# Performance work log

Hardware: AMD Instinct MI355X
Metric: run time of the kernel (lower is better)

Reference implementation:

```python
import jax, jax.numpy as jnp
import numpy as np

N = 50000
E = 800000
IN_C, HID, HEADS, CLS = 128, 64, 5, 40
NEG_SLOPE = 0.2


def gat_conv(h, src, dst, W, a_src, a_dst, bias, heads, out_c, concat):
    n = h.shape[0]
    hp = (h @ W).reshape(n, heads, out_c)            # [N,H,C]
    a_s = jnp.sum(hp * a_src, axis=-1)               # [N,H]
    a_d = jnp.sum(hp * a_dst, axis=-1)               # [N,H]
    e = jax.nn.leaky_relu(a_s[src] + a_d[dst], NEG_SLOPE)  # [Etot,H]
    m = jax.ops.segment_max(e, dst, num_segments=n)  # segment softmax over dst
    e = jnp.exp(e - m[dst])
    s = jax.ops.segment_sum(e, dst, num_segments=n)
    alpha = e / (s[dst] + 1e-16)                     # [Etot,H]
    msg = hp[src] * alpha[:, :, None]                # [Etot,H,C]
    out = jax.ops.segment_sum(msg, dst, num_segments=n)
    if concat:
        out = out.reshape(n, heads * out_c)
    else:
        out = out.mean(axis=1)
    return out + bias


def setup_inputs() -> dict:
    key = jax.random.key(0)
    ks = jax.random.split(key, 12)
    x = jax.random.normal(ks[0], (N, IN_C), dtype=jnp.float32)
    edge_index = jax.random.randint(ks[1], (2, E), 0, N, dtype=jnp.int64)
    g = 0.1
    return {
        "x": x,
        "edge_index": edge_index,
        "emb_W": jax.random.normal(ks[2], (IN_C, HID), jnp.float32) * g,
        "emb_b": jnp.zeros((HID,), jnp.float32),
        "W1": jax.random.normal(ks[3], (HID, HEADS * HID), jnp.float32) * g,
        "att_src1": jax.random.normal(ks[4], (HEADS, HID), jnp.float32) * g,
        "att_dst1": jax.random.normal(ks[5], (HEADS, HID), jnp.float32) * g,
        "b1": jnp.zeros((HEADS * HID,), jnp.float32),
        "W2": jax.random.normal(ks[6], (HEADS * HID, HEADS * CLS), jnp.float32) * g,
        "att_src2": jax.random.normal(ks[7], (HEADS, CLS), jnp.float32) * g,
        "att_dst2": jax.random.normal(ks[8], (HEADS, CLS), jnp.float32) * g,
        "b2": jnp.zeros((CLS,), jnp.float32),
    }


def reference(x, edge_index, emb_W, emb_b, W1, att_src1, att_dst1, b1,
              W2, att_src2, att_dst2, b2):
    n = x.shape[0]
    loops = jnp.arange(n, dtype=edge_index.dtype)
    src = jnp.concatenate([edge_index[0], loops])  # PyG adds self-loops
    dst = jnp.concatenate([edge_index[1], loops])
    h = x @ emb_W + emb_b
    emb = h
    # dropout skipped (eval mode)
    h = jax.nn.elu(gat_conv(h, src, dst, W1, att_src1, att_dst1, b1, HEADS, HID, True))
    h = gat_conv(h, src, dst, W2, att_src2, att_dst2, b2, HEADS, CLS, False)
    return emb, jax.nn.log_softmax(h, axis=1)
```

## Files before the change

### kernel.cpp

```cpp
#include <hip/hip_runtime.h>
#include <math.h>

constexpr int N_NODES = 50000;
constexpr int E_EDGES = 800000;
constexpr int ETOT    = E_EDGES + N_NODES;
constexpr int IN_C    = 128;
constexpr int HID     = 64;
constexpr int HEADS   = 5;
constexpr int CLS     = 40;
constexpr int SLOTW   = 96;
constexpr int CSTR    = 16;
constexpr float NEG_SLOPE = 0.2f;

typedef __attribute__((ext_vector_type(8))) short short8;
typedef __attribute__((ext_vector_type(4))) float float4v;
typedef __attribute__((ext_vector_type(2))) float f32x2;

__device__ __forceinline__ float lrelu(float v) {
    return v > 0.f ? v : NEG_SLOPE * v;
}
__device__ __forceinline__ float bf2f(unsigned short u) {
    return __uint_as_float(((unsigned)u) << 16);
}
__device__ __forceinline__ f32x2 bfp2f(unsigned u) {
    f32x2 r;
    r.x = __uint_as_float(u << 16);
    r.y = __uint_as_float(u & 0xFFFF0000u);
    return r;
}
__device__ __forceinline__ unsigned short f2bf(float f) {
    unsigned u = __float_as_uint(f);
    return (unsigned short)((u + 0x7fffu + ((u >> 16) & 1u)) >> 16);
}

__device__ __forceinline__ void pack_one(const float* __restrict__ B,
                                         unsigned short* __restrict__ Bp,
                                         int N, int KS, int t)
{
    int lane = t & 63;
    int f = (t >> 6) & 3;
    int rest = t >> 8;
    int ks = rest % KS;
    int nt = rest / KS;
    int n = nt * 64 + f * 16 + (lane & 15);
    int kbase = ks * 32 + (lane >> 4) * 8;
    unsigned short vals[8];
    #pragma unroll
    for (int j = 0; j < 8; j++) {
        float v = (n < N) ? B[(long)(kbase + j) * N + n] : 0.f;
        vals[j] = f2bf(v);
    }
    *(ushort4*)(Bp + (long)t * 8)     = make_ushort4(vals[0], vals[1], vals[2], vals[3]);
    *(ushort4*)(Bp + (long)t * 8 + 4) = make_ushort4(vals[4], vals[5], vals[6], vals[7]);
}

__global__ void pack_weights(const float* __restrict__ W0, const float* __restrict__ W1,
                             const float* __restrict__ W2,
                             const float* __restrict__ att1s, const float* __restrict__ att1d,
                             const float* __restrict__ att2s, const float* __restrict__ att2d,
                             unsigned short* __restrict__ Bp0,
                             unsigned short* __restrict__ Bp1,
                             unsigned short* __restrict__ Bp2,
                             float* __restrict__ u1s, float* __restrict__ u1d,
                             unsigned short* __restrict__ Bs,
                             int* __restrict__ cnt, unsigned short* __restrict__ slots)
{
    int t = blockIdx.x * blockDim.x + threadIdx.x;
    if (t < 13824) {
        if (t < 1024)      pack_one(W0, Bp0, 64,  4,  t);
        else if (t < 3584) pack_one(W1, Bp1, 320, 2,  t - 1024);
        else               pack_one(W2, Bp2, 200, 10, t - 3584);
    } else if (t < 14464) {
        int i = t - 13824;
        bool isd = i >= 320;
        int j = isd ? i - 320 : i;
        int h = j >> 6, k = j & 63;
        const float* att = isd ? att1d : att1s;
        float sum = 0.f;
        for (int c = 0; c < 64; c++)
            sum += W1[k * 320 + h * 64 + c] * att[h * 64 + c];
        (isd ? u1d : u1s)[j] = sum;
    } else if (t < 15104) {
        int i = t - 14464;
        int lane = i & 63, ks = i >> 6;
        int n = lane & 15, kq = lane >> 4;
        unsigned short vals[8];
        #pragma unroll
        for (int j = 0; j < 8; j++) {
            int k = ks * 32 + kq * 8 + j;
            float sum = 0.f;
            if (n < 5) {
                for (int c = 0; c < 40; c++)
                    sum += W2[k * 200 + n * 40 + c] * att2s[n * 40 + c];
            } else if (n >= 8 && n < 13) {
                int h = n - 8;
                for (int c = 0; c < 40; c++)
                    sum += W2[k * 200 + h * 40 + c] * att2d[h * 40 + c];
            }
            vals[j] = f2bf(sum);
        }
        *(ushort4*)(Bs + (long)i * 8)     = make_ushort4(vals[0], vals[1], vals[2], vals[3]);
        *(ushort4*)(Bs + (long)i * 8 + 4) = make_ushort4(vals[4], vals[5], vals[6], vals[7]);
    }
    if (t < N_NODES) {
        cnt[t * CSTR] = 1;
        slots[t * SLOTW] = (unsigned short)t;
    }
}

__global__ __launch_bounds__(256) void emb_scatter_fused(
    const float* __restrict__ A, const unsigned short* __restrict__ Bp,
    const float* __restrict__ bias,
    const float* __restrict__ u1s, const float* __restrict__ u1d,
    float* __restrict__ Cf, unsigned short* __restrict__ Cb,
    float* __restrict__ asd, int M,
    const int* __restrict__ ei, int* __restrict__ cnt,
    unsigned short* __restrict__ slots, int nScat)
{
    if ((int)blockIdx.x < nScat) {
        int base = blockIdx.x * 1024 + threadIdx.x;
        int s[4], d[4], pos[4];
        bool ok[4];
        #pragma unroll
        for (int j = 0; j < 4; j++) {
            int t = base + j * 256;
            ok[j] = t < E_EDGES;
            int tt = ok[j] ? t : 0;
            s[j] = ei[tt];
            d[j] = ei[E_EDGES + tt];
        }
        #pragma unroll
        for (int j = 0; j < 4; j++)
            pos[j] = ok[j] ? atomicAdd(&cnt[d[j] * CSTR], 1) : SLOTW;
        #pragma unroll
        for (int j = 0; j < 4; j++)
            if (pos[j] < SLOTW)
                slots[d[j] * SLOTW + pos[j]] = (unsigned short)s[j];
        return;
    }
    const int gb = blockIdx.x - nScat;
    const int K = 128, KS = 4;
    const int w = threadIdx.x >> 6, lane = threadIdx.x & 63;
    const int cl = lane & 15, kq = lane >> 4;
    int rowA = gb * 64 + w * 16 + cl;
    if (rowA >= M) rowA = M - 1;
    const float* ap = A + (long)rowA * K + kq * 8;
    const unsigned short* bp = Bp + lane * 8;
    float4v acc[4] = {};
    #pragma unroll
    for (int ks = 0; ks < KS; ks++) {
        float4 u0 = *(const float4*)(ap + ks * 32);
        float4 u1 = *(const float4*)(ap + ks * 32 + 4);
        short8 a;
        a[0] = f2bf(u0.x); a[1] = f2bf(u0.y); a[2] = f2bf(u0.z); a[3] = f2bf(u0.w);
        a[4] = f2bf(u1.x); a[5] = f2bf(u1.y); a[6] = f2bf(u1.z); a[7] = f2bf(u1.w);
        #pragma unroll
        for (int f = 0; f < 4; f++) {
            short8 b = *(const short8*)(bp + ks * 2048 + f * 512);
            acc[f] = __builtin_amdgcn_mfma_f32_16x16x32_bf16(a, b, acc[f], 0, 0, 0);
        }
    }
    int rbase = gb * 64 + w * 16 + kq * 4;
    float bc4[4];
    #pragma unroll
    for (int f = 0; f < 4; f++) {
        int col = f * 16 + cl;
        float bc = bias[col];
        bc4[f] = bc;
        #pragma unroll
        for (int r = 0; r < 4; r++) {
            int row = rbase + r;
            if (row < M) {
                float v = acc[f][r] + bc;
                Cf[(long)row * 64 + col] = v;
                Cb[(long)row * 64 + col] = f2bf(v);
            }
        }
    }
    #pragma unroll
    for (int h = 0; h < HEADS; h++) {
        float us[4], ud[4];
        #pragma unroll
        for (int f = 0; f < 4; f++) {
            us[f] = u1s[h * 64 + f * 16 + cl];
            ud[f] = u1d[h * 64 + f * 16 + cl];
        }
        #pragma unroll
        for (int r = 0; r < 4; r++) {
            float ps = 0.f, pd = 0.f;
            #pragma unroll
            for (int f = 0; f < 4; f++) {
                float v = acc[f][r] + bc4[f];
                ps += v * us[f];
                pd += v * ud[f];
            }
            #pragma unroll
            for (int off = 1; off < 16; off <<= 1) {
                ps += __shfl_xor(ps, off);
                pd += __shfl_xor(pd, off);
            }
            int row = rbase + r;
            if (cl == 0 && row < M) {
                asd[row * 16 + h]     = ps;
                asd[row * 16 + 8 + h] = pd;
            }
        }
    }
}

__global__ __launch_bounds__(256) void aggr1_new(
    const int* __restrict__ cnt, const unsigned short* __restrict__ slots,
    const float* __restrict__ asd,
    const unsigned short* __restrict__ emb, unsigned short* __restrict__ e_out)
{
    __shared__ float alph[4][64 * 8];
    int wid = (blockIdx.x * blockDim.x + threadIdx.x) >> 6;
    int w = threadIdx.x >> 6;
    int lane = threadIdx.x & 63;
    if (wid >= N_NODES) return;
    int deg = cnt[wid * CSTR];
    if (deg > SLOTW) deg = SLOTW;
    const unsigned short* myslot = slots + wid * SLOTW;

    float adh[HEADS];
    #pragma unroll
    for (int h = 0; h < HEADS; h++) adh[h] = asd[wid * 16 + 8 + h];

    const char* embB = (const char*)emb;

    if (deg <= 64) {
        bool has = lane < deg;
        int s = has ? (int)myslot[lane] : 0;
        int rowoff = s * 128;
        float4 s4 = *(const float4*)(asd + s * 16);
        float  s5 = asd[s * 16 + 4];
        float v[HEADS], sm[HEADS];
        v[0] = has ? __expf(lrelu(s4.x + adh[0])) : 0.f;
        v[1] = has ? __expf(lrelu(s4.y + adh[1])) : 0.f;
        v[2] = has ? __expf(lrelu(s4.z + adh[2])) : 0.f;
        v[3] = has ? __expf(lrelu(s4.w + adh[3])) : 0.f;
        v[4] = has ? __expf(lrelu(s5   + adh[4])) : 0.f;
        #pragma unroll
        for (int h = 0; h < HEADS; h++) sm[h] = v[h];
        if (deg <= 32) {
            #pragma unroll
            for (int h = 0; h < HEADS; h++)
                #pragma unroll
                for (int off = 16; off; off >>= 1)
                    sm[h] += __shfl_xor(sm[h], off);
        } else {
            #pragma unroll
            for (int h = 0; h < HEADS; h++)
                #pragma unroll
                for (int off = 32; off; off >>= 1)
                    sm[h] += __shfl_xor(sm[h], off);
        }
        #pragma unroll
        for (int h = 0; h < HEADS; h++)
            alph[w][lane * 8 + h] = v[h] / (sm[h] + 1e-16f);

        const int g = lane >> 4, cl16 = lane & 15;
        f32x2 av[HEADS][2] = {};
        int nE8 = (deg + 7) & ~7;
        for (int i = 0; i < nE8; i += 8) {
            int e0 = i + g, e1 = i + 4 + g;
            int off0 = __shfl(rowoff, e0);
            int off1 = __shfl(rowoff, e1);
            uint2 q0 = *(const uint2*)(embB + off0 + cl16 * 8);
            uint2 q1 = *(const uint2*)(embB + off1 + cl16 * 8);
            float4 b0 = *(const float4*)&alph[w][e0 * 8];
            float  b4 = alph[w][e0 * 8 + 4];
            float4 c0 = *(const float4*)&alph[w][e1 * 8];
            float  c4 = alph[w][e1 * 8 + 4];
            f32x2 f0a = bfp2f(q0.x), f0b = bfp2f(q0.y);
            f32x2 f1a = bfp2f(q1.x), f1b = bfp2f(q1.y);
            av[0][0] += f0a * b0.x; av[0][1] += f0b * b0.x;
            av[1][0] += f0a * b0.y; av[1][1] += f0b * b0.y;
            av[2][0] += f0a * b0.z; av[2][1] += f0b * b0.z;
            av[3][0] += f0a * b0.w; av[3][1] += f0b * b0.w;
            av[4][0] += f0a * b4;   av[4][1] += f0b * b4;
            av[0][0] += f1a * c0.x; av[0][1] += f1b * c0.x;
            av[1][0] += f1a * c0.y; av[1][1] += f1b * c0.y;
            av[2][0] += f1a * c0.z; av[2][1] += f1b * c0.z;
            av[3][0] += f1a * c0.w; av[3][1] += f1b * c0.w;
            av[4][0] += f1a * c4;   av[4][1] += f1b * c4;
        }
        #pragma unroll
        for (int h = 0; h < HEADS; h++)
            #pragma unroll
            for (int p = 0; p < 2; p++) {
                float tx = av[h][p].x, ty = av[h][p].y;
                tx += __shfl_xor(tx, 16); tx += __shfl_xor(tx, 32);
                ty += __shfl_xor(ty, 16); ty += __shfl_xor(ty, 32);
                av[h][p].x = tx; av[h][p].y = ty;
            }
        if (g == 0) {
            #pragma unroll
            for (int h = 0; h < HEADS; h++) {
                ushort4 o = make_ushort4(f2bf(av[h][0].x), f2bf(av[h][0].y),
                                         f2bf(av[h][1].x), f2bf(av[h][1].y));
                *(ushort4*)(e_out + (long)wid * 320 + h * 64 + cl16 * 4) = o;
            }
        }
    } else {
        float acc[HEADS] = {};
        float inv[HEADS], sm[HEADS] = {};
        for (int e = lane; e < deg; e += 64) {
            int s = myslot[e];
            #pragma unroll
            for (int h = 0; h < HEADS; h++)
                sm[h] += __expf(lrelu(asd[s * 16 + h] + adh[h]));
        }
        #pragma unroll
        for (int h = 0; h < HEADS; h++) {
            #pragma unroll
            for (int off = 32; off; off >>= 1)
                sm[h] += __shfl_xor(sm[h], off);
            inv[h] = 1.f / (sm[h] + 1e-16f);
        }
        for (int e = 0; e < deg; e++) {
            int s0 = myslot[e];
            float fv = bf2f(*(const unsigned short*)(embB + s0 * 128 + lane * 2));
            #pragma unroll
            for (int h = 0; h < HEADS; h++) {
                float a0 = __expf(lrelu(asd[s0 * 16 + h] + adh[h])) * inv[h];
                acc[h] += fv * a0;
            }
        }
        #pragma unroll
        for (int h = 0; h < HEADS; h++)
            e_out[(long)wid * 320 + h * 64 + lane] = f2bf(acc[h]);
    }
}

__global__ __launch_bounds__(256, 5) void gemm_mix_l2(
    const unsigned short* __restrict__ A, const unsigned short* __restrict__ Bp1,
    const unsigned short* __restrict__ Bp2, const float* __restrict__ bias,
    const unsigned short* __restrict__ Bs,
    unsigned short* __restrict__ hp2, float* __restrict__ asd, int M)
{
    constexpr int LDP = 328;
    __shared__ unsigned short tile[32 * LDP];
    const int wid = threadIdx.x >> 6, lane = threadIdx.x & 63;
    const int band = wid >> 1, half = wid & 1;
    const int cl = lane & 15, kq = lane >> 4;
    int rowA = blockIdx.x * 32 + band * 16 + cl;
    if (rowA >= M) rowA = M - 1;
    const unsigned short* ap = A + (long)rowA * 320;
    const unsigned short* bp1 = Bp1 + lane * 8;

    const int rbase = blockIdx.x * 32 + band * 16 + kq * 4;
    const int lrow = band * 16 + kq * 4;

    if (half == 0) {
        float4v acc[12] = {};
        #pragma unroll
        for (int i = 0; i < 3; i++)
            #pragma unroll
            for (int ks = 0; ks < 2; ks++) {
                short8 a = *(const short8*)(ap + i * 64 + ks * 32 + kq * 8);
                #pragma unroll
                for (int f = 0; f < 4; f++) {
                    short8 b = *(const short8*)(bp1 + (i * 2 + ks) * 2048 + f * 512);
                    acc[i * 4 + f] =
                        __builtin_amdgcn_mfma_f32_16x16x32_bf16(a, b, acc[i * 4 + f], 0, 0, 0);
                }
            }
        #pragma unroll
        for (int i = 0; i < 3; i++)
            #pragma unroll
            for (int f = 0; f < 4; f++) {
                int col = i * 64 + f * 16 + cl;
                float bc = bias[col];
                #pragma unroll
                for (int r = 0; r < 4; r++) {
                    float v = acc[i * 4 + f][r] + bc;
                    v = v > 0.f ? v : __expf(v) - 1.f;
                    tile[(lrow + r) * LDP + col] = f2bf(v);
                }
            }
    } else {
        float4v acc[8] = {};
        #pragma unroll
        for (int i = 0; i < 2; i++)
            #pragma unroll
            for (int ks = 0; ks < 2; ks++) {
                short8 a = *(const short8*)(ap + (3 + i) * 64 + ks * 32 + kq * 8);
                #pragma unroll
                for (int f = 0; f < 4; f++) {
                    short8 b = *(const short8*)(bp1 + ((3 + i) * 2 + ks) * 2048 + f * 512);
                    acc[i * 4 + f] =
                        __builtin_amdgcn_mfma_f32_16x16x32_bf16(a, b, acc[i * 4 + f], 0, 0, 0);
                }
            }
        #pragma unroll
        for (int i = 0; i < 2; i++)
            #pragma unroll
            for (int f = 0; f < 4; f++) {
                int col = (3 + i) * 64 + f * 16 + cl;
                float bc = bias[col];
                #pragma unroll
                for (int r = 0; r < 4; r++) {
                    float v = acc[i * 4 + f][r] + bc;
                    v = v > 0.f ? v : __expf(v) - 1.f;
                    tile[(lrow + r) * LDP + col] = f2bf(v);
                }
            }
    }
    __syncthreads();

    const unsigned short* arow = tile + (band * 16 + cl) * LDP;
    const unsigned short* bp2 = Bp2 + lane * 8;
    const unsigned short* bs  = Bs + lane * 8;
    float4v acc2[8] = {};
    float4v accs = {};
    #pragma unroll
    for (int ks = 0; ks < 10; ks++) {
        short8 a2 = *(const short8*)(arow + ks * 32 + kq * 8);
        if (half == 0) {
            short8 b = *(const short8*)(bs + ks * 512);
            accs = __builtin_amdgcn_mfma_f32_16x16x32_bf16(a2, b, accs, 0, 0, 0);
        }
        #pragma unroll
        for (int nt2 = 0; nt2 < 2; nt2++)
            #pragma unroll
            for (int f = 0; f < 4; f++) {
                short8 b = *(const short8*)(bp2 + (((half * 2 + nt2) * 10 + ks) * 2048) + f * 512);
                acc2[nt2 * 4 + f] =
                    __builtin_amdgcn_mfma_f32_16x16x32_bf16(a2, b, acc2[nt2 * 4 + f], 0, 0, 0);
            }
    }
    if (half == 0) {
        #pragma unroll
        for (int r = 0; r < 4; r++) {
            int row = rbase + r;
            if (row < M) asd[row * 16 + cl] = accs[r];
        }
    }
    #pragma unroll
    for (int nt2 = 0; nt2 < 2; nt2++)
        #pragma unroll
        for (int f = 0; f < 4; f++) {
            int col = (half * 2 + nt2) * 64 + f * 16 + cl;
            if (col >= 200) continue;
            #pragma unroll
            for (int r = 0; r < 4; r++) {
                int row = rbase + r;
                if (row < M) hp2[(long)row * 200 + col] = f2bf(acc2[nt2 * 4 + f][r]);
            }
        }
}

__global__ __launch_bounds__(256) void aggr2_fused(
    const int* __restrict__ cnt, const unsigned short* __restrict__ slots,
    const float* __restrict__ asd,
    const unsigned short* __restrict__ hp, const float* __restrict__ bias,
    float* __restrict__ out)
{
    __shared__ float alph[4][320];
    int wid = (blockIdx.x * blockDim.x + threadIdx.x) >> 6;
    int w = threadIdx.x >> 6;
    int lane = threadIdx.x & 63;
    if (wid >= N_NODES) return;
    int deg = cnt[wid * CSTR];
    if (deg > SLOTW) deg = SLOTW;
    const unsigned short* myslot = slots + wid * SLOTW;

    float adh[HEADS];
    #pragma unroll
    for (int h = 0; h < HEADS; h++) adh[h] = asd[wid * 16 + 8 + h];

    const bool act = lane < 50;
    const int ch4 = lane * 4;
    const int hq  = act ? lane / 10 : 0;
    const char* hpB = (const char*)hp;
    f32x2 acc01 = {0.f, 0.f}, acc23 = {0.f, 0.f};

    if (deg <= 64) {
        bool has = lane < deg;
        int s = has ? (int)myslot[lane] : 0;
        int rowoff = s * 400;
        float4 s4 = *(const float4*)(asd + s * 16);
        float  s5 = asd[s * 16 + 4];
        float v[HEADS], sm[HEADS];
        v[0] = has ? __expf(lrelu(s4.x + adh[0])) : 0.f;
        v[1] = has ? __expf(lrelu(s4.y + adh[1])) : 0.f;
        v[2] = has ? __expf(lrelu(s4.z + adh[2])) : 0.f;
        v[3] = has ? __expf(lrelu(s4.w + adh[3])) : 0.f;
        v[4] = has ? __expf(lrelu(s5   + adh[4])) : 0.f;
        #pragma unroll
        for (int h = 0; h < HEADS; h++) sm[h] = v[h];
        if (deg <= 32) {
            #pragma unroll
            for (int h = 0; h < HEADS; h++)
                #pragma unroll
                for (int off = 16; off; off >>= 1)
                    sm[h] += __shfl_xor(sm[h], off);
        } else {
            #pragma unroll
            for (int h = 0; h < HEADS; h++)
                #pragma unroll
                for (int off = 32; off; off >>= 1)
                    sm[h] += __shfl_xor(sm[h], off);
        }
        if (has) {
            #pragma unroll
            for (int h = 0; h < HEADS; h++)
                alph[w][lane * 5 + h] = 0.2f * v[h] / (sm[h] + 1e-16f);
        }
        int i = 0;
        for (; i + 7 < deg; i += 8) {
            uint2 q[8]; float a[8];
            #pragma unroll
            for (int k = 0; k < 8; k++) {
                int off = __shfl(rowoff, i + k);
                q[k] = act ? *(const uint2*)(hpB + off + ch4 * 2)
                           : make_uint2(0u, 0u);
                a[k] = alph[w][(i + k) * 5 + hq];
            }
            #pragma unroll
            for (int k = 0; k < 8; k++) {
                f32x2 fa = bfp2f(q[k].x), fb = bfp2f(q[k].y);
                acc01 += fa * a[k];
                acc23 += fb * a[k];
            }
        }
        for (; i < deg; i++) {
            int off = __shfl(rowoff, i);
            if (act) {
                uint2 q0 = *(const uint2*)(hpB + off + ch4 * 2);
                float a0 = alph[w][i * 5 + hq];
                f32x2 fa = bfp2f(q0.x), fb = bfp2f(q0.y);
                acc01 += fa * a0;
                acc23 += fb * a0;
            }
        }
    } else {
        float inv[HEADS], sm[HEADS] = {};
        for (int e = lane; e < deg; e += 64) {
            int s = myslot[e];
            #pragma unroll
            for (int h = 0; h < HEADS; h++)
                sm[h] += __expf(lrelu(asd[s * 16 + h] + adh[h]));
        }
        #pragma unroll
        for (int h = 0; h < HEADS; h++) {
            #pragma unroll
            for (int off = 32; off; off >>= 1)
                sm[h] += __shfl_xor(sm[h], off);
            inv[h] = 0.2f / (sm[h] + 1e-16f);
        }
        for (int e = 0; e < deg; e++) {
            int s0 = myslot[e];
            if (act) {
                uint2 q0 = *(const uint2*)(hpB + s0 * 400 + ch4 * 2);
                float a0 = __expf(lrelu(asd[s0 * 16 + hq] + adh[hq])) * inv[hq];
                f32x2 fa = bfp2f(q0.x), fb = bfp2f(q0.y);
                acc01 += fa * a0;
                acc23 += fb * a0;
            }
        }
    }

    if (act)
        *(float4*)&alph[w][lane * 4] =
            make_float4(acc01.x, acc01.y, acc23.x, acc23.y);
    float vb0 = -1e30f, vb1 = -1e30f, vb2 = -1e30f, vb3 = -1e30f;
    if (lane < 10) {
        float r0 = 0.f, r1 = 0.f, r2 = 0.f, r3 = 0.f;
        #pragma unroll
        for (int h = 0; h < HEADS; h++) {
            float4 t = *(const float4*)&alph[w][(lane + 10 * h) * 4];
            r0 += t.x; r1 += t.y; r2 += t.z; r3 += t.w;
        }
        vb0 = r0 + bias[ch4 + 0];
        vb1 = r1 + bias[ch4 + 1];
        vb2 = r2 + bias[ch4 + 2];
        vb3 = r3 + bias[ch4 + 3];
    }
    float mxv = fmaxf(fmaxf(vb0, vb1), fmaxf(vb2, vb3));
    #pragma unroll
    for (int off = 8; off; off >>= 1)
        mxv = fmaxf(mxv, __shfl_xor(mxv, off));
    float sme = 0.f;
    if (lane < 10)
        sme = __expf(vb0 - mxv) + __expf(vb1 - mxv) +
              __expf(vb2 - mxv) + __expf(vb3 - mxv);
    #pragma unroll
    for (int off = 8; off; off >>= 1)
        sme += __shfl_xor(sme, off);
    float ls = mxv + __logf(sme);
    if (lane < 10) {
        float4 o = make_float4(vb0 - ls, vb1 - ls, vb2 - ls, vb3 - ls);
        *(float4*)(out + (long)wid * CLS + ch4) = o;
    }
}

extern "C" void kernel_launch(void* const* d_in, const int* in_sizes, int n_in,
                              void* d_out, int out_size, void* d_ws, size_t ws_size,
                              hipStream_t stream)
{
    const float* x     = (const float*)d_in[0];
    const int*   ei    = (const int*)d_in[1];
    const float* emb_W = (const float*)d_in[2];
    const float* emb_b = (const float*)d_in[3];
    const float* W1    = (const float*)d_in[4];
    const float* as1   = (const float*)d_in[5];
    const float* ad1   = (const float*)d_in[6];
    const float* b1    = (const float*)d_in[7];
    const float* W2    = (const float*)d_in[8];
    const float* as2   = (const float*)d_in[9];
    const float* ad2   = (const float*)d_in[10];
    const float* b2    = (const float*)d_in[11];

    float* out_emb = (float*)d_out;
    float* out_cls = (float*)d_out + (size_t)N_NODES * HID;

    char* ws = (char*)d_ws;
    unsigned short* e_agg  = (unsigned short*)(ws);
    unsigned short* hp2b   = (unsigned short*)(ws + 32000000);
    float*          asd1   = (float*)(ws + 52000000);
    float*          asd2   = (float*)(ws + 55200000);
    int*            cnt    = (int*)(ws + 58400000);
    unsigned short* embb   = (unsigned short*)(ws + 64000000);
    unsigned short* Bp0    = (unsigned short*)(ws + 74400000);
    unsigned short* Bp1    = (unsigned short*)(ws + 74500000);
    unsigned short* Bp2    = (unsigned short*)(ws + 74600000);
    float*          u1s    = (float*)(ws + 74800000);
    float*          u1d    = (float*)(ws + 74810000);
    unsigned short* Bs     = (unsigned short*)(ws + 74820000);
    unsigned short* slots  = (unsigned short*)(ws + 75100000);

    const dim3 blk(256);
    const int nb4  = (N_NODES + 3) / 4;
    const int mgrid  = (N_NODES + 63) / 64;
    const int mgrid2 = (N_NODES + 31) / 32;
    const int nScat  = (E_EDGES + 1023) / 1024;
    const int pgrid  = (N_NODES + 255) / 256;

    pack_weights<<<pgrid, blk, 0, stream>>>(emb_W, W1, W2, as1, ad1, as2, ad2,
                                            Bp0, Bp1, Bp2, u1s, u1d, Bs,
                                            cnt, slots);

    emb_scatter_fused<<<nScat + mgrid, blk, 0, stream>>>(
        x, Bp0, emb_b, u1s, u1d, out_emb, embb, asd1, N_NODES,
        ei, cnt, slots, nScat);

    aggr1_new<<<nb4, blk, 0, stream>>>(cnt, slots, asd1, embb, e_agg);

    gemm_mix_l2<<<mgrid2, blk, 0, stream>>>(e_agg, Bp1, Bp2, b1, Bs,
                                            hp2b, asd2, N_NODES);

    aggr2_fused<<<nb4, blk, 0, stream>>>(cnt, slots, asd2, hp2b, b2, out_cls);
}
```

Before: 314.6 us.

## Process two destination nodes per wavefront in layer-2 aggregation

Reworks the layer-2 aggregation so each 64-lane wavefront handles a pair of nodes, one node per 32-lane half, whenever both degrees are at most 32. Each active lane now gathers 16-byte chunks of the source rows, so 25 lanes cover the 200 bf16 channels instead of 50 lanes with 8-byte loads. The aim is to fill the idle lanes and halve the number of wavefronts, since degrees average about 17. Pairs where either node has more than 32 edges fall back to the old path run sequentially for both nodes, and each half's loop runs to the larger of the two degrees.

```diff
diff --git a/kernel.cpp b/kernel.cpp
--- a/kernel.cpp
+++ b/kernel.cpp
@@ -458,27 +458,28 @@
     float* __restrict__ out)
 {
     __shared__ float alph[4][320];
-    int wid = (blockIdx.x * blockDim.x + threadIdx.x) >> 6;
-    int w = threadIdx.x >> 6;
-    int lane = threadIdx.x & 63;
-    if (wid >= N_NODES) return;
-    int deg = cnt[wid * CSTR];
-    if (deg > SLOTW) deg = SLOTW;
-    const unsigned short* myslot = slots + wid * SLOTW;
-
-    float adh[HEADS];
-    #pragma unroll
-    for (int h = 0; h < HEADS; h++) adh[h] = asd[wid * 16 + 8 + h];
-
-    const bool act = lane < 50;
-    const int ch4 = lane * 4;
-    const int hq  = act ? lane / 10 : 0;
+    __shared__ float part[4][400];
+    const int w = threadIdx.x >> 6;
+    const int lane = threadIdx.x & 63;
+    const int half = lane >> 5, l32 = lane & 31;
+    const int pairId = blockIdx.x * 4 + w;
+    if (pairId * 2 >= N_NODES) return;
     const char* hpB = (const char*)hp;
-    f32x2 acc01 = {0.f, 0.f}, acc23 = {0.f, 0.f};
-
-    if (deg <= 64) {
-        bool has = lane < deg;
-        int s = has ? (int)myslot[lane] : 0;
+
+    int nodeF = pairId * 2 + half;
+    int degF = cnt[nodeF * CSTR];
+    if (degF > SLOTW) degF = SLOTW;
+    int degO = __shfl_xor(degF, 32);
+    int degMax = degF > degO ? degF : degO;
+
+    if (degMax <= 32) {
+        const unsigned short* myslot = slots + nodeF * SLOTW;
+        float adh[HEADS];
+        #pragma unroll
+        for (int h = 0; h < HEADS; h++) adh[h] = asd[nodeF * 16 + 8 + h];
+
+        bool has = l32 < degF;
+        int s = has ? (int)myslot[l32] : 0;
         int rowoff = s * 400;
         float4 s4 = *(const float4*)(asd + s * 16);
         float  s5 = asd[s * 16 + 4];
@@ -490,109 +491,202 @@
         v[4] = has ? __expf(lrelu(s5   + adh[4])) : 0.f;
         #pragma unroll
         for (int h = 0; h < HEADS; h++) sm[h] = v[h];
-        if (deg <= 32) {
-            #pragma unroll
-            for (int h = 0; h < HEADS; h++)
-                #pragma unroll
-                for (int off = 16; off; off >>= 1)
-                    sm[h] += __shfl_xor(sm[h], off);
-        } else {
+        #pragma unroll
+        for (int h = 0; h < HEADS; h++)
+            #pragma unroll
+            for (int off = 16; off; off >>= 1)
+                sm[h] += __shfl_xor(sm[h], off);
+        float* al = &alph[w][half * 160];
+        #pragma unroll
+        for (int h = 0; h < HEADS; h++)
+            al[l32 * 5 + h] = 0.2f * v[h] / (sm[h] + 1e-16f);
+
+        const bool act = l32 < 25;
+        const int hq = l32 / 5, cg = l32 % 5;
+        const int choff = hq * 80 + cg * 16;
+        f32x2 ac[4] = {};
+        int nE8 = (degMax + 7) & ~7;
+        for (int i = 0; i < nE8; i += 8) {
+            uint4 q[8]; float a[8];
+            #pragma unroll
+            for (int k = 0; k < 8; k++) {
+                int e = i + k;
+                int off = __shfl(rowoff, e, 32);
+                q[k] = act ? *(const uint4*)(hpB + off + choff)
+                           : make_uint4(0u, 0u, 0u, 0u);
+                a[k] = al[e * 5 + hq];
+            }
+            #pragma unroll
+            for (int k = 0; k < 8; k++) {
+                ac[0] += bfp2f(q[k].x) * a[k];
+                ac[1] += bfp2f(q[k].y) * a[k];
+                ac[2] += bfp2f(q[k].z) * a[k];
+                ac[3] += bfp2f(q[k].w) * a[k];
+            }
+        }
+        float* pt = &part[w][half * 200];
+        if (act) {
+            *(float4*)&pt[l32 * 8]     = make_float4(ac[0].x, ac[0].y, ac[1].x, ac[1].y);
+            *(float4*)&pt[l32 * 8 + 4] = make_float4(ac[2].x, ac[2].y, ac[3].x, ac[3].y);
+        }
+        float vb0 = -1e30f, vb1 = -1e30f, vb2 = -1e30f, vb3 = -1e30f;
+        if (l32 < 10) {
+            int cgr = l32 >> 1, j0 = (l32 & 1) * 4;
+            float4 r = make_float4(0.f, 0.f, 0.f, 0.f);
+            #pragma unroll
+            for (int h = 0; h < HEADS; h++) {
+                float4 t = *(const float4*)&pt[(h * 5 + cgr) * 8 + j0];
+                r.x += t.x; r.y += t.y; r.z += t.z; r.w += t.w;
+            }
+            vb0 = r.x + bias[l32 * 4 + 0];
+            vb1 = r.y + bias[l32 * 4 + 1];
+            vb2 = r.z + bias[l32 * 4 + 2];
+            vb3 = r.w + bias[l32 * 4 + 3];
+        }
+        float mxv = fmaxf(fmaxf(vb0, vb1), fmaxf(vb2, vb3));
+        #pragma unroll
+        for (int off = 8; off; off >>= 1)
+            mxv = fmaxf(mxv, __shfl_xor(mxv, off));
+        float sme = 0.f;
+        if (l32 < 10)
+            sme = __expf(vb0 - mxv) + __expf(vb1 - mxv) +
+                  __expf(vb2 - mxv) + __expf(vb3 - mxv);
+        #pragma unroll
+        for (int off = 8; off; off >>= 1)
+            sme += __shfl_xor(sme, off);
+        float ls = mxv + __logf(sme);
+        if (l32 < 10) {
+            float4 o = make_float4(vb0 - ls, vb1 - ls, vb2 - ls, vb3 - ls);
+            *(float4*)(out + (long)nodeF * CLS + l32 * 4) = o;
+        }
+        return;
+    }
+
+    for (int t = 0; t < 2; t++) {
+        int wid2 = pairId * 2 + t;
+        int deg = cnt[wid2 * CSTR];
+        if (deg > SLOTW) deg = SLOTW;
+        const unsigned short* myslot = slots + wid2 * SLOTW;
+
+        float adh[HEADS];
+        #pragma unroll
+        for (int h = 0; h < HEADS; h++) adh[h] = asd[wid2 * 16 + 8 + h];
+
+        const bool act = lane < 50;
+        const int ch4 = lane * 4;
+        const int hq  = act ? lane / 10 : 0;
+        f32x2 acc01 = {0.f, 0.f}, acc23 = {0.f, 0.f};
+
+        if (deg <= 64) {
+            bool has = lane < deg;
+            int s = has ? (int)myslot[lane] : 0;
+            int rowoff = s * 400;
+            float4 s4 = *(const float4*)(asd + s * 16);
+            float  s5 = asd[s * 16 + 4];
+            float v[HEADS], sm[HEADS];
+            v[0] = has ? __expf(lrelu(s4.x + adh[0])) : 0.f;
+            v[1] = has ? __expf(lrelu(s4.y + adh[1])) : 0.f;
+            v[2] = has ? __expf(lrelu(s4.z + adh[2])) : 0.f;
+            v[3] = has ? __expf(lrelu(s4.w + adh[3])) : 0.f;
+            v[4] = has ? __expf(lrelu(s5   + adh[4])) : 0.f;
+            #pragma unroll
+            for (int h = 0; h < HEADS; h++) sm[h] = v[h];
             #pragma unroll
             for (int h = 0; h < HEADS; h++)
                 #pragma unroll
                 for (int off = 32; off; off >>= 1)
                     sm[h] += __shfl_xor(sm[h], off);
-        }
-        if (has) {
-            #pragma unroll
-            for (int h = 0; h < HEADS; h++)
-                alph[w][lane * 5 + h] = 0.2f * v[h] / (sm[h] + 1e-16f);
-        }
-        int i = 0;
-        for (; i + 7 < deg; i += 8) {
-            uint2 q[8]; float a[8];
-            #pragma unroll
-            for (int k = 0; k < 8; k++) {
-                int off = __shfl(rowoff, i + k);
-                q[k] = act ? *(const uint2*)(hpB + off + ch4 * 2)
-                           : make_uint2(0u, 0u);
-                a[k] = alph[w][(i + k) * 5 + hq];
-            }
-            #pragma unroll
-            for (int k = 0; k < 8; k++) {
-                f32x2 fa = bfp2f(q[k].x), fb = bfp2f(q[k].y);
-                acc01 += fa * a[k];
-                acc23 += fb * a[k];
-            }
-        }
-        for (; i < deg; i++) {
-            int off = __shfl(rowoff, i);
-            if (act) {
-                uint2 q0 = *(const uint2*)(hpB + off + ch4 * 2);
-                float a0 = alph[w][i * 5 + hq];
-                f32x2 fa = bfp2f(q0.x), fb = bfp2f(q0.y);
-                acc01 += fa * a0;
-                acc23 += fb * a0;
-            }
-        }
-    } else {
-        float inv[HEADS], sm[HEADS] = {};
-        for (int e = lane; e < deg; e += 64) {
-            int s = myslot[e];
-            #pragma unroll
-            for (int h = 0; h < HEADS; h++)
-                sm[h] += __expf(lrelu(asd[s * 16 + h] + adh[h]));
-        }
-        #pragma unroll
-        for (int h = 0; h < HEADS; h++) {
-            #pragma unroll
-            for (int off = 32; off; off >>= 1)
-                sm[h] += __shfl_xor(sm[h], off);
-            inv[h] = 0.2f / (sm[h] + 1e-16f);
-        }
-        for (int e = 0; e < deg; e++) {
-            int s0 = myslot[e];
-            if (act) {
-                uint2 q0 = *(const uint2*)(hpB + s0 * 400 + ch4 * 2);
-                float a0 = __expf(lrelu(asd[s0 * 16 + hq] + adh[hq])) * inv[hq];
-                f32x2 fa = bfp2f(q0.x), fb = bfp2f(q0.y);
-                acc01 += fa * a0;
-                acc23 += fb * a0;
-            }
-        }
-    }
-
-    if (act)
-        *(float4*)&alph[w][lane * 4] =
-            make_float4(acc01.x, acc01.y, acc23.x, acc23.y);
-    float vb0 = -1e30f, vb1 = -1e30f, vb2 = -1e30f, vb3 = -1e30f;
-    if (lane < 10) {
-        float r0 = 0.f, r1 = 0.f, r2 = 0.f, r3 = 0.f;
-        #pragma unroll
-        for (int h = 0; h < HEADS; h++) {
-            float4 t = *(const float4*)&alph[w][(lane + 10 * h) * 4];
-            r0 += t.x; r1 += t.y; r2 += t.z; r3 += t.w;
-        }
-        vb0 = r0 + bias[ch4 + 0];
-        vb1 = r1 + bias[ch4 + 1];
-        vb2 = r2 + bias[ch4 + 2];
-        vb3 = r3 + bias[ch4 + 3];
-    }
-    float mxv = fmaxf(fmaxf(vb0, vb1), fmaxf(vb2, vb3));
-    #pragma unroll
-    for (int off = 8; off; off >>= 1)
-        mxv = fmaxf(mxv, __shfl_xor(mxv, off));
-    float sme = 0.f;
-    if (lane < 10)
-        sme = __expf(vb0 - mxv) + __expf(vb1 - mxv) +
-              __expf(vb2 - mxv) + __expf(vb3 - mxv);
-    #pragma unroll
-    for (int off = 8; off; off >>= 1)
-        sme += __shfl_xor(sme, off);
-    float ls = mxv + __logf(sme);
-    if (lane < 10) {
-        float4 o = make_float4(vb0 - ls, vb1 - ls, vb2 - ls, vb3 - ls);
-        *(float4*)(out + (long)wid * CLS + ch4) = o;
+            if (has) {
+                #pragma unroll
+                for (int h = 0; h < HEADS; h++)
+                    alph[w][lane * 5 + h] = 0.2f * v[h] / (sm[h] + 1e-16f);
+            }
+            int i = 0;
+            for (; i + 7 < deg; i += 8) {
+                uint2 q[8]; float a[8];
+                #pragma unroll
+                for (int k = 0; k < 8; k++) {
+                    int off = __shfl(rowoff, i + k);
+                    q[k] = act ? *(const uint2*)(hpB + off + ch4 * 2)
+                               : make_uint2(0u, 0u);
+                    a[k] = alph[w][(i + k) * 5 + hq];
+                }
+                #pragma unroll
+                for (int k = 0; k < 8; k++) {
+                    f32x2 fa = bfp2f(q[k].x), fb = bfp2f(q[k].y);
+                    acc01 += fa * a[k];
+                    acc23 += fb * a[k];
+                }
+            }
+            for (; i < deg; i++) {
+                int off = __shfl(rowoff, i);
+                if (act) {
+                    uint2 q0 = *(const uint2*)(hpB + off + ch4 * 2);
+                    float a0 = alph[w][i * 5 + hq];
+                    f32x2 fa = bfp2f(q0.x), fb = bfp2f(q0.y);
+                    acc01 += fa * a0;
+                    acc23 += fb * a0;
+                }
+            }
+        } else {
+            float inv[HEADS], sm[HEADS] = {};
+            for (int e = lane; e < deg; e += 64) {
+                int s = myslot[e];
+                #pragma unroll
+                for (int h = 0; h < HEADS; h++)
+                    sm[h] += __expf(lrelu(asd[s * 16 + h] + adh[h]));
+            }
+            #pragma unroll
+            for (int h = 0; h < HEADS; h++) {
+                #pragma unroll
+                for (int off = 32; off; off >>= 1)
+                    sm[h] += __shfl_xor(sm[h], off);
+                inv[h] = 0.2f / (sm[h] + 1e-16f);
+            }
+            for (int e = 0; e < deg; e++) {
+                int s0 = myslot[e];
+                if (act) {
+                    uint2 q0 = *(const uint2*)(hpB + s0 * 400 + ch4 * 2);
+                    float a0 = __expf(lrelu(asd[s0 * 16 + hq] + adh[hq])) * inv[hq];
+                    f32x2 fa = bfp2f(q0.x), fb = bfp2f(q0.y);
+                    acc01 += fa * a0;
+                    acc23 += fb * a0;
+                }
+            }
+        }
+
+        if (act)
+            *(float4*)&part[w][lane * 4] =
+                make_float4(acc01.x, acc01.y, acc23.x, acc23.y);
+        float vb0 = -1e30f, vb1 = -1e30f, vb2 = -1e30f, vb3 = -1e30f;
+        if (lane < 10) {
+            float r0 = 0.f, r1 = 0.f, r2 = 0.f, r3 = 0.f;
+            #pragma unroll
+            for (int h = 0; h < HEADS; h++) {
+                float4 tt = *(const float4*)&part[w][(lane + 10 * h) * 4];
+                r0 += tt.x; r1 += tt.y; r2 += tt.z; r3 += tt.w;
+            }
+            vb0 = r0 + bias[ch4 + 0];
+            vb1 = r1 + bias[ch4 + 1];
+            vb2 = r2 + bias[ch4 + 2];
+            vb3 = r3 + bias[ch4 + 3];
+        }
+        float mxv = fmaxf(fmaxf(vb0, vb1), fmaxf(vb2, vb3));
+        #pragma unroll
+        for (int off = 8; off; off >>= 1)
+            mxv = fmaxf(mxv, __shfl_xor(mxv, off));
+        float sme = 0.f;
+        if (lane < 10)
+            sme = __expf(vb0 - mxv) + __expf(vb1 - mxv) +
+                  __expf(vb2 - mxv) + __expf(vb3 - mxv);
+        #pragma unroll
+        for (int off = 8; off; off >>= 1)
+            sme += __shfl_xor(sme, off);
+        float ls = mxv + __logf(sme);
+        if (lane < 10) {
+            float4 o = make_float4(vb0 - ls, vb1 - ls, vb2 - ls, vb3 - ls);
+            *(float4*)(out + (long)wid2 * CLS + ch4) = o;
+        }
     }
 }
 
@@ -637,6 +731,8 @@
     const int mgrid2 = (N_NODES + 31) / 32;
     const int nScat  = (E_EDGES + 1023) / 1024;
     const int pgrid  = (N_NODES + 255) / 256;
+    const int npair  = (N_NODES + 1) / 2;
+    const int nb8    = (npair + 3) / 4;
 
     pack_weights<<<pgrid, blk, 0, stream>>>(emb_W, W1, W2, as1, ad1, as2, ad2,
                                             Bp0, Bp1, Bp2, u1s, u1d, Bs,
@@ -651,5 +747,5 @@
     gemm_mix_l2<<<mgrid2, blk, 0, stream>>>(e_agg, Bp1, Bp2, b1, Bs,
                                             hp2b, asd2, N_NODES);
 
-    aggr2_fused<<<nb4, blk, 0, stream>>>(cnt, slots, asd2, hp2b, b2, out_cls);
-}
+    aggr2_fused<<<nb8, blk, 0, stream>>>(cnt, slots, asd2, hp2b, b2, out_cls);
+}
```

Result: no change. 313.1 us (-0.5%).
